# Optimization experiments

Hardware: AMD Instinct MI355X
Metric: run time of the kernel (lower is better)

Reference implementation:

```python
import jax, jax.numpy as jnp
import numpy as np
from jax.ops import segment_sum

N_NODES = 50000
N_EDGES = 800000
IN_DIM, HID_DIM, OUT_DIM = 128, 128, 64
N_GRAPHS = 64


def setup_inputs() -> dict:
    key = jax.random.key(0)
    ks = jax.random.split(key, 8)
    x = jax.random.normal(ks[0], (N_NODES, IN_DIM), dtype=jnp.float32)
    edge_index = jax.random.randint(ks[1], (2, N_EDGES), 0, N_NODES, dtype=jnp.int64)
    batch = jnp.sort(jax.random.randint(ks[2], (N_NODES,), 0, N_GRAPHS, dtype=jnp.int64))
    # Glorot-ish init for GCNConv linear weights, zero bias (PyG default)
    W1 = jax.random.normal(ks[3], (IN_DIM, HID_DIM), dtype=jnp.float32) / np.sqrt(IN_DIM)
    b1 = jnp.zeros((HID_DIM,), dtype=jnp.float32)
    W2 = jax.random.normal(ks[4], (HID_DIM, OUT_DIM), dtype=jnp.float32) / np.sqrt(HID_DIM)
    b2 = jnp.zeros((OUT_DIM,), dtype=jnp.float32)
    return {"x": x, "W1": W1, "b1": b1, "W2": W2, "b2": b2,
            "edge_index": edge_index, "batch": batch, "num_graphs": N_GRAPHS}


def _gcn_conv(h, W, b, src, dst, deg_inv_sqrt, n_nodes):
    # h: [N, Fin] -> [N, Fout]; GCNConv: D^{-1/2}(A+I)D^{-1/2} (h W) + b
    hw = h @ W                                   # [N, Fout]
    norm = deg_inv_sqrt[src] * deg_inv_sqrt[dst] # [E]
    msg = hw[src] * norm[:, None]                # [E, Fout] (gather)
    agg = segment_sum(msg, dst, num_segments=n_nodes)  # scatter-add
    # self-loop contribution: norm_ii = deg_inv_sqrt[i]^2
    agg = agg + hw * (deg_inv_sqrt * deg_inv_sqrt)[:, None]
    return agg + b


def reference(x, W1, b1, W2, b2, edge_index, batch, num_graphs):
    n_nodes = x.shape[0]
    src, dst = edge_index[0], edge_index[1]
    # degree of A + I (self-loops added, as in PyG GCNConv default)
    deg = segment_sum(jnp.ones_like(dst, dtype=x.dtype), dst,
                      num_segments=n_nodes) + 1.0
    deg_inv_sqrt = jax.lax.rsqrt(deg)

    h = jax.nn.relu(_gcn_conv(x, W1, b1, src, dst, deg_inv_sqrt, n_nodes))
    h = jax.nn.relu(_gcn_conv(h, W2, b2, src, dst, deg_inv_sqrt, n_nodes))

    # global_mean_pool over batch ids
    sums = segment_sum(h, batch, num_segments=num_graphs)          # [G, Fout]
    counts = segment_sum(jnp.ones((n_nodes,), dtype=h.dtype), batch,
                         num_segments=num_graphs)                  # [G]
    return sums / jnp.maximum(counts, 1.0)[:, None]
```

## Files before the change

### kernel.cpp

```cpp
#include <hip/hip_runtime.h>

typedef float f4 __attribute__((ext_vector_type(4)));
typedef float f2 __attribute__((ext_vector_type(2)));
typedef short s8 __attribute__((ext_vector_type(8)));

union FU { unsigned u[4]; s8 s; };

__device__ __forceinline__ unsigned cvtpk(float lo, float hi){
  unsigned r;
  asm("v_cvt_pk_bf16_f32 %0, %1, %2" : "=v"(r) : "v"(lo), "v"(hi));
  return r;
}

__device__ __forceinline__ float bflo(unsigned v){ return __uint_as_float(v << 16); }
__device__ __forceinline__ float bfhi(unsigned v){ return __uint_as_float(v & 0xFFFF0000u); }

__device__ __forceinline__ int ld_idx(const void* p, int i, int is64){
  if (is64) return (int)((const long long*)p)[i];
  return ((const int*)p)[i];
}

__device__ __forceinline__ int detect64(const unsigned* __restrict__ e_raw, int e){
  int lane = threadIdx.x & 63;
  int lim = (e < 1024) ? e : 1024;
  int nz = 0;
  for (int i = lane; i < lim; i += 64) nz |= (e_raw[2*i + 1] != 0u);
  return (__ballot(nz != 0) == 0ull) ? 1 : 0;
}

template<int NC, int BIN>
__device__ __forceinline__ void gemm_body(const void* __restrict__ Xv,
                                          const float* __restrict__ W,
                                          unsigned short* __restrict__ Yb,
                                          int n, int blk, char* Alds){
  constexpr int NCF = NC/16;
  constexpr int WPC = 8/NCF;
  constexpr int RT  = 8/WPC;
  const int tid  = threadIdx.x;
  const int wave = tid >> 6, lane = tid & 63;
  const int rb = blk * 128;

  const int cbase = (wave % NCF) * 16;
  const int rt0   = (wave / NCF) * RT;
  const int col   = cbase + (lane & 15);
  const int kr0   = (lane >> 4) * 8;
  FU bu[4];
#pragma unroll
  for (int ks = 0; ks < 4; ++ks){
    float wv[8];
#pragma unroll
    for (int j = 0; j < 8; ++j) wv[j] = W[(size_t)(ks*32 + kr0 + j)*NC + col];
#pragma unroll
    for (int q = 0; q < 4; ++q) bu[ks].u[q] = cvtpk(wv[2*q], wv[2*q+1]);
  }

  for (int i = tid; i < 128*32; i += 512){
    int row = i >> 5, kq = i & 31;
    int rsrc = rb + row; if (rsrc >= n) rsrc = n - 1;
    uint2 dw;
    if (BIN){
      dw = ((const uint2*)Xv)[(size_t)rsrc*32 + kq];
    } else {
      f4 xv = ((const f4*)Xv)[(size_t)rsrc*32 + kq];
      dw = make_uint2(cvtpk(xv[0], xv[1]), cvtpk(xv[2], xv[3]));
    }
    int byte = (row*256 + kq*8) ^ ((row & 7) << 4);
    *reinterpret_cast<uint2*>(Alds + byte) = dw;
  }
  __syncthreads();

  f4 acc[RT];
#pragma unroll
  for (int rt = 0; rt < RT; ++rt) acc[rt] = 0.0f;

#pragma unroll
  for (int rt = 0; rt < RT; ++rt){
    const int arow = (rt0 + rt)*16 + (lane & 15);
#pragma unroll
    for (int ks = 0; ks < 4; ++ks){
      int kb = ks*32 + kr0;
      int byte = (arow*256 + kb*2) ^ ((arow & 7) << 4);
      s8 a = *reinterpret_cast<const s8*>(Alds + byte);
      acc[rt] = __builtin_amdgcn_mfma_f32_16x16x32_bf16(a, bu[ks].s, acc[rt], 0, 0, 0);
    }
  }

#pragma unroll
  for (int rt = 0; rt < RT; ++rt){
    int rowb = rb + (rt0 + rt)*16 + 4*(lane >> 4);
#pragma unroll
    for (int r = 0; r < 4; ++r){
      int row = rowb + r;
      if (row < n) Yb[(size_t)row*NC + col] = (unsigned short)cvtpk(acc[rt][r], acc[rt][r]);
    }
  }
}

template<int NC, int BIN>
__global__ __launch_bounds__(512) void gemm_k(const void* __restrict__ X,
                                              const float* __restrict__ W,
                                              unsigned short* __restrict__ Yb, int n){
  __shared__ int4 AldsV[2048];
  gemm_body<NC, BIN>(X, W, Yb, n, blockIdx.x, (char*)AldsV);
}

__global__ __launch_bounds__(512) void fused1_k(const float* __restrict__ X,
                                                const float* __restrict__ W1,
                                                unsigned short* __restrict__ Yb,
                                                const void* __restrict__ eidx,
                                                const void* __restrict__ batchp,
                                                int* __restrict__ counts,
                                                unsigned* __restrict__ etmp,
                                                int* __restrict__ batch32,
                                                int n, int e, int GB, int CB){
  __shared__ int4 AldsV[2048];
  __shared__ int hist[512];
  int blk = blockIdx.x;
  if (blk < GB){
    gemm_body<128, 0>(X, W1, Yb, n, blk, (char*)AldsV);
    return;
  }
  blk -= GB;
  const int NBK = (n + 127) >> 7;
  for (int i = threadIdx.x; i < NBK; i += 512) hist[i] = 0;
  __syncthreads();
  int is64 = detect64((const unsigned*)eidx, e);
  int CHK = (e + CB - 1) / CB;
  int beg = blk*CHK, end = min(e, beg + CHK);
  for (int i = beg + (int)threadIdx.x; i < end; i += 512){
    int s = ld_idx(eidx, i, is64);
    int d = ld_idx(eidx, e + i, is64);
    atomicAdd(&hist[d >> 7], 1);
    etmp[i] = (unsigned)s | ((unsigned)(d & 127) << 16) | ((unsigned)(d >> 7) << 23);
  }
  __syncthreads();
  for (int i = threadIdx.x; i < NBK; i += 512) counts[i*CB + blk] = hist[i];
  for (int i = blk*512 + (int)threadIdx.x; i < n; i += CB*512)
    batch32[i] = ld_idx(batchp, i, is64);
}

__global__ void scanA_k(const int* __restrict__ counts, int* __restrict__ base,
                        int* __restrict__ bsum, int L,
                        const int* __restrict__ batch32, float* __restrict__ invc,
                        float* __restrict__ out, int n, int g){
  __shared__ int sh[256];
  __shared__ int starts[257];
  int tid = threadIdx.x;
  int i = blockIdx.x*256 + tid;
  int v = (i < L) ? counts[i] : 0;
  sh[tid] = v; __syncthreads();
  for (int off = 1; off < 256; off <<= 1){
    int t = (tid >= off) ? sh[tid - off] : 0;
    __syncthreads();
    sh[tid] += t;
    __syncthreads();
  }
  if (i < L) base[i] = sh[tid] - v;
  if (tid == 255) bsum[blockIdx.x] = sh[255];
  if (blockIdx.x == 0){
    if (tid <= g){
      int lo = 0, hi = n;
      while (lo < hi){ int mid = (lo + hi) >> 1; if (batch32[mid] < tid) lo = mid + 1; else hi = mid; }
      starts[tid] = lo;
    }
    __syncthreads();
    if (tid < g){
      float c = (float)(starts[tid + 1] - starts[tid]);
      invc[tid] = 1.0f / fmaxf(c, 1.0f);
    }
    for (int k = tid; k < (g << 6); k += 256) out[k] = 0.0f;
  }
}

__global__ __launch_bounds__(512) void scat_k(const unsigned* __restrict__ etmp,
                                              const int* __restrict__ base,
                                              const int* __restrict__ bsum,
                                              int* __restrict__ bsumS,
                                              int* __restrict__ packed,
                                              int n, int e, int CB){
  __shared__ int sh[512];
  __shared__ int cur[512];
  int blk = blockIdx.x, tid = threadIdx.x;
  const int NBK = (n + 127) >> 7;
  int v = (tid < NBK) ? bsum[tid] : 0;
  sh[tid] = v; __syncthreads();
  for (int o = 1; o < 512; o <<= 1){
    int t = (tid >= o) ? sh[tid - o] : 0;
    __syncthreads();
    sh[tid] += t;
    __syncthreads();
  }
  int ex = sh[tid] - v;
  if (tid < NBK) cur[tid] = ex + base[tid*CB + blk];
  if (blk == 0){
    if (tid < NBK) bsumS[tid] = ex;
    if (tid == NBK - 1) bsumS[NBK] = sh[tid];
  }
  __syncthreads();
  int CHK = (e + CB - 1) / CB;
  int beg = blk*CHK, end = min(e, beg + CHK);
  for (int i = beg + tid; i < end; i += 512){
    unsigned w = etmp[i];
    int pos = atomicAdd(&cur[w >> 23], 1);
    packed[pos] = (int)(w & 0x7FFFFFu);
  }
}

#define CSR_CAP 6144
__global__ __launch_bounds__(256) void csr_k(const int* __restrict__ packed,
                                             const int* __restrict__ bsumS,
                                             int* __restrict__ esrcS,
                                             int* __restrict__ rowptr,
                                             float* __restrict__ dinv, int n, int e){
  __shared__ int vals[CSR_CAP];
  __shared__ int hist[128], off[128], cur[128];
  int b = blockIdx.x, tid = threadIdx.x;
  if (b == 0 && tid == 0) rowptr[n] = e;
  int sbeg = bsumS[b], send = bsumS[b + 1];
  int m = send - sbeg;
  int mL = min(m, CSR_CAP);
  for (int i = tid; i < mL; i += 256) vals[i] = packed[sbeg + i];
  if (tid < 128) hist[tid] = 0;
  __syncthreads();
  for (int i = tid; i < m; i += 256){
    int v = (i < CSR_CAP) ? vals[i] : packed[sbeg + i];
    atomicAdd(&hist[(v >> 16) & 127], 1);
  }
  __syncthreads();
  if (tid < 128) off[tid] = hist[tid];
  __syncthreads();
  for (int o = 1; o < 128; o <<= 1){
    int v = 0;
    if (tid < 128 && tid >= o) v = off[tid - o];
    __syncthreads();
    if (tid < 128) off[tid] += v;
    __syncthreads();
  }
  if (tid < 128){
    int ex = off[tid] - hist[tid];
    cur[tid] = ex;
    int node = b*128 + tid;
    if (node < n){
      rowptr[node] = sbeg + ex;
      dinv[node] = rsqrtf((float)hist[tid] + 1.0f);
    }
  }
  __syncthreads();
  for (int i = tid; i < m; i += 256){
    int v = (i < CSR_CAP) ? vals[i] : packed[sbeg + i];
    int pos = atomicAdd(&cur[(v >> 16) & 127], 1);
    esrcS[sbeg + pos] = v & 0xFFFF;
  }
}

__global__ __launch_bounds__(256) void agg128_k(const unsigned short* __restrict__ HWb,
                                                const float* __restrict__ dinv,
                                                const int* __restrict__ rowptr,
                                                const int* __restrict__ esrcS,
                                                const float* __restrict__ bias,
                                                unsigned short* __restrict__ Hb, int n){
  int wid  = (blockIdx.x*256 + threadIdx.x) >> 6;
  int lane = threadIdx.x & 63;
  if (wid >= n) return;
  wid = __builtin_amdgcn_readfirstlane(wid);
  const int slot = lane >> 4;
  const int cg   = lane & 15;
  float di = dinv[wid];
  float di2 = di * di;
  int beg = __builtin_amdgcn_readfirstlane(rowptr[wid]);
  int end = __builtin_amdgcn_readfirstlane(rowptr[wid + 1]);
  float acc[8];
#pragma unroll
  for (int k = 0; k < 8; ++k) acc[k] = 0.0f;
  const char* Hc = (const char*)HWb;
  int j = beg;
  for (; j + 16 <= end; j += 16){
    int s[4]; float wt[4]; uint4 v[4];
#pragma unroll
    for (int q = 0; q < 4; ++q) s[q] = esrcS[j + q*4 + slot];
#pragma unroll
    for (int q = 0; q < 4; ++q){
      wt[q] = dinv[s[q]] * di;
      v[q] = *(const uint4*)(Hc + (size_t)s[q]*256 + cg*16);
    }
#pragma unroll
    for (int q = 0; q < 4; ++q){
      acc[0] += bflo(v[q].x)*wt[q]; acc[1] += bfhi(v[q].x)*wt[q];
      acc[2] += bflo(v[q].y)*wt[q]; acc[3] += bfhi(v[q].y)*wt[q];
      acc[4] += bflo(v[q].z)*wt[q]; acc[5] += bfhi(v[q].z)*wt[q];
      acc[6] += bflo(v[q].w)*wt[q]; acc[7] += bfhi(v[q].w)*wt[q];
    }
  }
  for (; j < end; j += 4){
    int idx = j + slot;
    int live = (idx < end);
    if (!live) idx = end - 1;
    int s = esrcS[idx];
    float wt = live ? (dinv[s] * di) : 0.0f;
    uint4 v = *(const uint4*)(Hc + (size_t)s*256 + cg*16);
    acc[0] += bflo(v.x)*wt; acc[1] += bfhi(v.x)*wt;
    acc[2] += bflo(v.y)*wt; acc[3] += bfhi(v.y)*wt;
    acc[4] += bflo(v.z)*wt; acc[5] += bfhi(v.z)*wt;
    acc[6] += bflo(v.w)*wt; acc[7] += bfhi(v.w)*wt;
  }
#pragma unroll
  for (int k = 0; k < 8; ++k){
    acc[k] += __shfl_xor(acc[k], 16);
    acc[k] += __shfl_xor(acc[k], 32);
  }
  uint4 sv = *(const uint4*)(Hc + (size_t)wid*256 + cg*16);
  acc[0] += bflo(sv.x)*di2; acc[1] += bfhi(sv.x)*di2;
  acc[2] += bflo(sv.y)*di2; acc[3] += bfhi(sv.y)*di2;
  acc[4] += bflo(sv.z)*di2; acc[5] += bfhi(sv.z)*di2;
  acc[6] += bflo(sv.w)*di2; acc[7] += bfhi(sv.w)*di2;
  f4 b0 = *(const f4*)(bias + cg*8);
  f4 b1 = *(const f4*)(bias + cg*8 + 4);
#pragma unroll
  for (int k = 0; k < 4; ++k) acc[k] = fmaxf(acc[k] + b0[k], 0.0f);
#pragma unroll
  for (int k = 0; k < 4; ++k) acc[4+k] = fmaxf(acc[4+k] + b1[k], 0.0f);
  if (slot == 0){
    uint4 o;
    o.x = cvtpk(acc[0], acc[1]); o.y = cvtpk(acc[2], acc[3]);
    o.z = cvtpk(acc[4], acc[5]); o.w = cvtpk(acc[6], acc[7]);
    *(uint4*)((char*)Hb + (size_t)wid*256 + cg*16) = o;
  }
}

__global__ __launch_bounds__(512) void agg64p_k(const unsigned short* __restrict__ HWb,
                                                const float* __restrict__ dinv,
                                                const int* __restrict__ rowptr,
                                                const int* __restrict__ esrcS,
                                                const float* __restrict__ bias,
                                                const int* __restrict__ batch32,
                                                const float* __restrict__ invc,
                                                float* __restrict__ out, int n){
  __shared__ float h2s[8][64];
  __shared__ int bts[8];
  const int tid  = threadIdx.x;
  const int wave = tid >> 6;
  const int lane = tid & 63;
  int wid = blockIdx.x*8 + wave;
  const bool valid = (wid < n);
  if (!valid) wid = n - 1;
  wid = __builtin_amdgcn_readfirstlane(wid);
  const int slot = lane >> 3;
  const int cg   = lane & 7;
  float di = dinv[wid];
  float di2 = di * di;
  int beg = __builtin_amdgcn_readfirstlane(rowptr[wid]);
  int end = __builtin_amdgcn_readfirstlane(rowptr[wid + 1]);
  float acc[8];
#pragma unroll
  for (int k = 0; k < 8; ++k) acc[k] = 0.0f;
  const char* Hc = (const char*)HWb;
  int j = beg;
  for (; j + 16 <= end; j += 16){
    int s[2]; float wt[2]; uint4 v[2];
#pragma unroll
    for (int q = 0; q < 2; ++q) s[q] = esrcS[j + q*8 + slot];
#pragma unroll
    for (int q = 0; q < 2; ++q){
      wt[q] = dinv[s[q]] * di;
      v[q] = *(const uint4*)(Hc + (size_t)s[q]*128 + cg*16);
    }
#pragma unroll
    for (int q = 0; q < 2; ++q){
      acc[0] += bflo(v[q].x)*wt[q]; acc[1] += bfhi(v[q].x)*wt[q];
      acc[2] += bflo(v[q].y)*wt[q]; acc[3] += bfhi(v[q].y)*wt[q];
      acc[4] += bflo(v[q].z)*wt[q]; acc[5] += bfhi(v[q].z)*wt[q];
      acc[6] += bflo(v[q].w)*wt[q]; acc[7] += bfhi(v[q].w)*wt[q];
    }
  }
  for (; j < end; j += 8){
    int idx = j + slot;
    int live = (idx < end);
    if (!live) idx = end - 1;
    int s = esrcS[idx];
    float wt = live ? (dinv[s] * di) : 0.0f;
    uint4 v = *(const uint4*)(Hc + (size_t)s*128 + cg*16);
    acc[0] += bflo(v.x)*wt; acc[1] += bfhi(v.x)*wt;
    acc[2] += bflo(v.y)*wt; acc[3] += bfhi(v.y)*wt;
    acc[4] += bflo(v.z)*wt; acc[5] += bfhi(v.z)*wt;
    acc[6] += bflo(v.w)*wt; acc[7] += bfhi(v.w)*wt;
  }
#pragma unroll
  for (int k = 0; k < 8; ++k){
    acc[k] += __shfl_xor(acc[k], 8);
    acc[k] += __shfl_xor(acc[k], 16);
    acc[k] += __shfl_xor(acc[k], 32);
  }
  uint4 sv = *(const uint4*)(Hc + (size_t)wid*128 + cg*16);
  acc[0] += bflo(sv.x)*di2; acc[1] += bfhi(sv.x)*di2;
  acc[2] += bflo(sv.y)*di2; acc[3] += bfhi(sv.y)*di2;
  acc[4] += bflo(sv.z)*di2; acc[5] += bfhi(sv.z)*di2;
  acc[6] += bflo(sv.w)*di2; acc[7] += bfhi(sv.w)*di2;
  f4 b0 = *(const f4*)(bias + cg*8);
  f4 b1 = *(const f4*)(bias + cg*8 + 4);
#pragma unroll
  for (int k = 0; k < 4; ++k) acc[k] = fmaxf(acc[k] + b0[k], 0.0f);
#pragma unroll
  for (int k = 0; k < 4; ++k) acc[4+k] = fmaxf(acc[4+k] + b1[k], 0.0f);
  if (slot == 0){
#pragma unroll
    for (int k = 0; k < 8; ++k) h2s[wave][cg*8 + k] = acc[k];
  }
  if (lane == 0) bts[wave] = valid ? batch32[wid] : -1;
  __syncthreads();
  if (wave == 0){
    float a = 0.0f;
    int gcur = bts[0];
#pragma unroll
    for (int t = 0; t < 8; ++t){
      int bt = bts[t];
      if (bt >= 0){
        if (bt != gcur){
          unsafeAtomicAdd(&out[gcur*64 + lane], a * invc[gcur]);
          a = 0.0f; gcur = bt;
        }
        a += h2s[t][lane];
      }
    }
    unsafeAtomicAdd(&out[gcur*64 + lane], a * invc[gcur]);
  }
}

extern "C" void kernel_launch(void* const* d_in, const int* in_sizes, int n_in,
                              void* d_out, int out_size, void* d_ws, size_t ws_size,
                              hipStream_t stream){
  const float* x    = (const float*)d_in[0];
  const float* W1   = (const float*)d_in[1];
  const float* b1   = (const float*)d_in[2];
  const float* W2   = (const float*)d_in[3];
  const float* b2   = (const float*)d_in[4];
  const void*  eidx = d_in[5];
  const void*  batchp = d_in[6];
  const int n = in_sizes[0] / 128;
  const int e = in_sizes[5] / 2;
  const int g = out_size / 64;
  float* out = (float*)d_out;

  const int NBK = (n + 127) >> 7;
  const int CB  = 256;
  const int GB  = (n + 127) / 128;
  const int L   = NBK * CB;

  char* w = (char*)d_ws;
  int* counts  = (int*)w;
  int* base    = counts + (size_t)L;
  int* bsum    = base + (size_t)L;
  int* bsumS   = bsum + NBK;
  int* rowptr  = bsumS + (NBK + 1);
  int* batch32 = rowptr + (n + 1);
  float* dinv  = (float*)(batch32 + n);
  float* invc  = dinv + n;
  unsigned* etmp = (unsigned*)(invc + g);
  int* packed  = (int*)(etmp + e);
  int* esrcS   = packed + e;
  size_t ofs = (size_t)((char*)(esrcS + e) - w);
  ofs = (ofs + 255) & ~(size_t)255;
  unsigned short* HWb = (unsigned short*)(w + ofs);
  size_t ofs2 = ofs + (size_t)n * 128 * 2;
  ofs2 = (ofs2 + 255) & ~(size_t)255;
  unsigned short* Hb = (unsigned short*)(w + ofs2);

  fused1_k<<<GB + CB, 512, 0, stream>>>(x, W1, HWb, eidx, batchp,
                                        counts, etmp, batch32, n, e, GB, CB);
  scanA_k<<<NBK, 256, 0, stream>>>(counts, base, bsum, L, batch32, invc, out, n, g);
  scat_k<<<CB, 512, 0, stream>>>(etmp, base, bsum, bsumS, packed, n, e, CB);
  csr_k<<<NBK, 256, 0, stream>>>(packed, bsumS, esrcS, rowptr, dinv, n, e);

  agg128_k<<<(n + 3)/4, 256, 0, stream>>>(HWb, dinv, rowptr, esrcS, b1, Hb, n);
  gemm_k<64, 1><<<GB, 512, 0, stream>>>(Hb, W2, HWb, n);
  agg64p_k<<<(n + 7)/8, 512, 0, stream>>>(HWb, dinv, rowptr, esrcS, b2,
                                          batch32, invc, out, n);
}
```

Before: 117.4 us.

## Fuse layer-2 GEMM into layer-1 aggregation kernel via LDS tile

The first-layer aggregation now runs 16 nodes per 1024-thread block and stages the ReLU'd bf16 hidden rows in shared memory. Four waves then multiply that 16x128 tile by W2 with MFMA and write HW2 directly, so the separate gemm_k launch and the global round trip of the hidden activations are gone. In exchange, every block reloads and converts W2 from global memory, the larger blocks add a barrier, and 12 of the 16 waves sit idle during the MFMA phase.

New measurement: 118.7 us. About the same (+1.1%).

```diff
diff --git a/kernel.cpp b/kernel.cpp
--- a/kernel.cpp
+++ b/kernel.cpp
@@ -28,22 +28,17 @@
   return (__ballot(nz != 0) == 0ull) ? 1 : 0;
 }
 
-template<int NC, int BIN>
-__device__ __forceinline__ void gemm_body(const void* __restrict__ Xv,
-                                          const float* __restrict__ W,
-                                          unsigned short* __restrict__ Yb,
-                                          int n, int blk, char* Alds){
-  constexpr int NCF = NC/16;
-  constexpr int WPC = 8/NCF;
-  constexpr int RT  = 8/WPC;
+__device__ __forceinline__ void gemm_body128(const float* __restrict__ Xv,
+                                             const float* __restrict__ W,
+                                             unsigned short* __restrict__ Yb,
+                                             int n, int blk, char* Alds){
+  constexpr int NC = 128;
   const int tid  = threadIdx.x;
   const int wave = tid >> 6, lane = tid & 63;
   const int rb = blk * 128;
 
-  const int cbase = (wave % NCF) * 16;
-  const int rt0   = (wave / NCF) * RT;
-  const int col   = cbase + (lane & 15);
-  const int kr0   = (lane >> 4) * 8;
+  const int col = wave * 16 + (lane & 15);
+  const int kr0 = (lane >> 4) * 8;
   FU bu[4];
 #pragma unroll
   for (int ks = 0; ks < 4; ++ks){
@@ -57,25 +52,20 @@
   for (int i = tid; i < 128*32; i += 512){
     int row = i >> 5, kq = i & 31;
     int rsrc = rb + row; if (rsrc >= n) rsrc = n - 1;
-    uint2 dw;
-    if (BIN){
-      dw = ((const uint2*)Xv)[(size_t)rsrc*32 + kq];
-    } else {
-      f4 xv = ((const f4*)Xv)[(size_t)rsrc*32 + kq];
-      dw = make_uint2(cvtpk(xv[0], xv[1]), cvtpk(xv[2], xv[3]));
-    }
+    f4 xv = ((const f4*)Xv)[(size_t)rsrc*32 + kq];
+    uint2 dw = make_uint2(cvtpk(xv[0], xv[1]), cvtpk(xv[2], xv[3]));
     int byte = (row*256 + kq*8) ^ ((row & 7) << 4);
     *reinterpret_cast<uint2*>(Alds + byte) = dw;
   }
   __syncthreads();
 
-  f4 acc[RT];
-#pragma unroll
-  for (int rt = 0; rt < RT; ++rt) acc[rt] = 0.0f;
-
-#pragma unroll
-  for (int rt = 0; rt < RT; ++rt){
-    const int arow = (rt0 + rt)*16 + (lane & 15);
+  f4 acc[8];
+#pragma unroll
+  for (int rt = 0; rt < 8; ++rt) acc[rt] = 0.0f;
+
+#pragma unroll
+  for (int rt = 0; rt < 8; ++rt){
+    const int arow = rt*16 + (lane & 15);
 #pragma unroll
     for (int ks = 0; ks < 4; ++ks){
       int kb = ks*32 + kr0;
@@ -86,22 +76,14 @@
   }
 
 #pragma unroll
-  for (int rt = 0; rt < RT; ++rt){
-    int rowb = rb + (rt0 + rt)*16 + 4*(lane >> 4);
+  for (int rt = 0; rt < 8; ++rt){
+    int rowb = rb + rt*16 + 4*(lane >> 4);
 #pragma unroll
     for (int r = 0; r < 4; ++r){
       int row = rowb + r;
       if (row < n) Yb[(size_t)row*NC + col] = (unsigned short)cvtpk(acc[rt][r], acc[rt][r]);
     }
   }
-}
-
-template<int NC, int BIN>
-__global__ __launch_bounds__(512) void gemm_k(const void* __restrict__ X,
-                                              const float* __restrict__ W,
-                                              unsigned short* __restrict__ Yb, int n){
-  __shared__ int4 AldsV[2048];
-  gemm_body<NC, BIN>(X, W, Yb, n, blockIdx.x, (char*)AldsV);
 }
 
 __global__ __launch_bounds__(512) void fused1_k(const float* __restrict__ X,
@@ -117,7 +99,7 @@
   __shared__ int hist[512];
   int blk = blockIdx.x;
   if (blk < GB){
-    gemm_body<128, 0>(X, W1, Yb, n, blk, (char*)AldsV);
+    gemm_body128(X, W1, Yb, n, blk, (char*)AldsV);
     return;
   }
   blk -= GB;
@@ -253,15 +235,21 @@
   }
 }
 
-__global__ __launch_bounds__(256) void agg128_k(const unsigned short* __restrict__ HWb,
-                                                const float* __restrict__ dinv,
-                                                const int* __restrict__ rowptr,
-                                                const int* __restrict__ esrcS,
-                                                const float* __restrict__ bias,
-                                                unsigned short* __restrict__ Hb, int n){
-  int wid  = (blockIdx.x*256 + threadIdx.x) >> 6;
-  int lane = threadIdx.x & 63;
-  if (wid >= n) return;
+__global__ __launch_bounds__(1024) void agg128mm_k(const unsigned short* __restrict__ HWb,
+                                                   const float* __restrict__ dinv,
+                                                   const int* __restrict__ rowptr,
+                                                   const int* __restrict__ esrcS,
+                                                   const float* __restrict__ bias,
+                                                   const float* __restrict__ W2,
+                                                   unsigned short* __restrict__ HW2b,
+                                                   int n){
+  __shared__ int4 h1l[256];
+  char* h1c = (char*)h1l;
+  const int tid  = threadIdx.x;
+  const int wave = tid >> 6;
+  const int lane = tid & 63;
+  int wid = blockIdx.x*16 + wave;
+  if (wid >= n) wid = n - 1;
   wid = __builtin_amdgcn_readfirstlane(wid);
   const int slot = lane >> 4;
   const int cg   = lane & 15;
@@ -323,7 +311,39 @@
     uint4 o;
     o.x = cvtpk(acc[0], acc[1]); o.y = cvtpk(acc[2], acc[3]);
     o.z = cvtpk(acc[4], acc[5]); o.w = cvtpk(acc[6], acc[7]);
-    *(uint4*)((char*)Hb + (size_t)wid*256 + cg*16) = o;
+    int byte = (wave*256 + cg*16) ^ ((wave & 7) << 4);
+    *reinterpret_cast<uint4*>(h1c + byte) = o;
+  }
+  __syncthreads();
+
+  if (wave < 4){
+    const int col = wave*16 + (lane & 15);
+    const int kr0 = (lane >> 4) * 8;
+    FU bu[4];
+#pragma unroll
+    for (int ks = 0; ks < 4; ++ks){
+      float wv[8];
+#pragma unroll
+      for (int jq = 0; jq < 8; ++jq) wv[jq] = W2[(size_t)(ks*32 + kr0 + jq)*64 + col];
+#pragma unroll
+      for (int q = 0; q < 4; ++q) bu[ks].u[q] = cvtpk(wv[2*q], wv[2*q+1]);
+    }
+    f4 c4 = 0.0f;
+    const int arow = lane & 15;
+#pragma unroll
+    for (int ks = 0; ks < 4; ++ks){
+      int kb = ks*32 + kr0;
+      int byte = (arow*256 + kb*2) ^ ((arow & 7) << 4);
+      s8 a = *reinterpret_cast<const s8*>(h1c + byte);
+      c4 = __builtin_amdgcn_mfma_f32_16x16x32_bf16(a, bu[ks].s, c4, 0, 0, 0);
+    }
+    int rowb = blockIdx.x*16 + 4*(lane >> 4);
+#pragma unroll
+    for (int r = 0; r < 4; ++r){
+      int row = rowb + r;
+      if (row < n)
+        HW2b[(size_t)row*64 + col] = (unsigned short)cvtpk(c4[r], c4[r]);
+    }
   }
 }
 
@@ -462,7 +482,7 @@
   unsigned short* HWb = (unsigned short*)(w + ofs);
   size_t ofs2 = ofs + (size_t)n * 128 * 2;
   ofs2 = (ofs2 + 255) & ~(size_t)255;
-  unsigned short* Hb = (unsigned short*)(w + ofs2);
+  unsigned short* HW2b = (unsigned short*)(w + ofs2);
 
   fused1_k<<<GB + CB, 512, 0, stream>>>(x, W1, HWb, eidx, batchp,
                                         counts, etmp, batch32, n, e, GB, CB);
@@ -470,8 +490,8 @@
   scat_k<<<CB, 512, 0, stream>>>(etmp, base, bsum, bsumS, packed, n, e, CB);
   csr_k<<<NBK, 256, 0, stream>>>(packed, bsumS, esrcS, rowptr, dinv, n, e);
 
-  agg128_k<<<(n + 3)/4, 256, 0, stream>>>(HWb, dinv, rowptr, esrcS, b1, Hb, n);
-  gemm_k<64, 1><<<GB, 512, 0, stream>>>(Hb, W2, HWb, n);
-  agg64p_k<<<(n + 7)/8, 512, 0, stream>>>(HWb, dinv, rowptr, esrcS, b2,
+  agg128mm_k<<<(n + 15)/16, 1024, 0, stream>>>(HWb, dinv, rowptr, esrcS, b1, W2,
+                                               HW2b, n);
+  agg64p_k<<<(n + 7)/8, 512, 0, stream>>>(HW2b, dinv, rowptr, esrcS, b2,
                                           batch32, invc, out, n);
 }
```
